# Performance work log

Measured on AMD Instinct MI355X. Metric: run time of the kernel, lower is better.

## Reference

```python
import jax, jax.numpy as jnp
import numpy as np

NUM_USERS = 100000
NUM_ITEMS = 200000
EMBED_DIM = 64
NUM_LAYERS = 3
NNZ = 4000000
BATCH = 16384
N_TOTAL = NUM_USERS + NUM_ITEMS


def setup_inputs() -> dict:
    key = jax.random.key(0)
    k = jax.random.split(key, 7)
    user_ids = jax.random.randint(k[0], (BATCH,), 0, NUM_USERS, dtype=jnp.int32)
    item_ids = jax.random.randint(k[1], (BATCH,), 0, NUM_ITEMS, dtype=jnp.int32)
    adj_row = jax.random.randint(k[2], (NNZ,), 0, N_TOTAL, dtype=jnp.int32)
    adj_col = jax.random.randint(k[3], (NNZ,), 0, N_TOTAL, dtype=jnp.int32)
    # normalized-adjacency-like positive values (D^-1/2 A D^-1/2 entries)
    adj_val = jax.random.uniform(k[4], (NNZ,), dtype=jnp.float32) * 0.1
    user_emb_w = jax.random.normal(k[5], (NUM_USERS, EMBED_DIM), dtype=jnp.float32) * 0.1
    item_emb_w = jax.random.normal(k[6], (NUM_ITEMS, EMBED_DIM), dtype=jnp.float32) * 0.1
    return {"user_ids": user_ids, "item_ids": item_ids, "adj_row": adj_row,
            "adj_col": adj_col, "adj_val": adj_val,
            "user_emb_w": user_emb_w, "item_emb_w": item_emb_w}


def _spmm(row, col, val, x):
    # y = A @ x for COO sparse A: gather source rows, scale, scatter-add to dest rows
    msgs = x[col] * val[:, None]  # [nnz, D]
    return jax.ops.segment_sum(msgs, row, num_segments=N_TOTAL)


def reference(user_ids, item_ids, adj_row, adj_col, adj_val, user_emb_w, item_emb_w):
    all_emb = jnp.concatenate([user_emb_w, item_emb_w], axis=0)  # [N+M, D]
    acc = all_emb  # running sum over K+1 layer embeddings (== stack+mean)
    x = all_emb
    for _ in range(NUM_LAYERS):
        x = _spmm(adj_row, adj_col, adj_val, x)
        acc = acc + x
    final = acc / jnp.float32(NUM_LAYERS + 1)
    u = final[user_ids]                    # [B, D]
    i = final[item_ids + NUM_USERS]        # [B, D]
    return jnp.sum(u * i, axis=-1)         # [B]
```

## Files before the change

### kernel.cpp

```cpp
#include <hip/hip_runtime.h>
#include <hip/hip_fp16.h>

#define NUM_USERS 100000
#define NUM_ITEMS 200000
#define NT        300000
#define D         64
#define NNZ_C     4000000
#define BATCH     16384

#define SB_LOG    10
#define SB_ROWS   1024
#define NSB       ((NT + SB_ROWS - 1) / SB_ROWS)
#define SBCAP     16384
#define CHUNK     8192
#define NCHUNK    ((NNZ_C + CHUNK - 1) / CHUNK)

__device__ inline void fma8(float4& a, float4& b, float v, uint4 g) {
    const __half2* h = (const __half2*)&g;
    float2 f0 = __half22float2(h[0]); a.x += v * f0.x; a.y += v * f0.y;
    float2 f1 = __half22float2(h[1]); a.z += v * f1.x; a.w += v * f1.y;
    float2 f2 = __half22float2(h[2]); b.x += v * f2.x; b.y += v * f2.y;
    float2 f3 = __half22float2(h[3]); b.z += v * f3.x; b.w += v * f3.y;
}

__device__ inline unsigned pack2(float x, float y) {
    __half2 h = __floats2half2_rn(x, y);
    return *(unsigned*)&h;
}

__global__ void p1_bin(const int* __restrict__ row, const int* __restrict__ col,
                       const float* __restrict__ val, int* __restrict__ bcnt,
                       int2* __restrict__ entries) {
    __shared__ int hist[NSB];
    __shared__ int cur[NSB];
    int tid = threadIdx.x;
    long cb = (long)blockIdx.x * CHUNK;
    int n = (int)((NNZ_C - cb < CHUNK) ? (NNZ_C - cb) : CHUNK);
    for (int i = tid; i < NSB; i += 512) hist[i] = 0;
    __syncthreads();
    for (int k = tid; k < n; k += 512)
        atomicAdd(&hist[row[cb + k] >> SB_LOG], 1);
    __syncthreads();
    for (int i = tid; i < NSB; i += 512)
        cur[i] = atomicAdd(&bcnt[i], hist[i]);
    __syncthreads();
    for (int k = tid; k < n; k += 512) {
        int r = row[cb + k];
        int b = r >> SB_LOG;
        int pos = atomicAdd(&cur[b], 1);
        if (pos < SBCAP)
            entries[(long)b * SBCAP + pos] =
                make_int2(col[cb + k] | ((r & (SB_ROWS - 1)) << 19),
                          __float_as_int(val[cb + k]));
    }
}

__global__ void bucket_scan(const int* __restrict__ bcnt, int* __restrict__ bucketstart,
                            int* __restrict__ rowstart) {
    __shared__ int s[512];
    int tid = threadIdx.x;
    int v = (tid < NSB) ? min(bcnt[tid], SBCAP) : 0;
    int acc = v;
    s[tid] = acc; __syncthreads();
    for (int off = 1; off < 512; off <<= 1) {
        int t = (tid >= off) ? s[tid - off] : 0;
        __syncthreads();
        acc += t; s[tid] = acc; __syncthreads();
    }
    if (tid < NSB) bucketstart[tid] = acc - v;
    if (tid == 0) rowstart[NT] = s[511];
}

__global__ void p2_csr(const int* __restrict__ bcnt, const int* __restrict__ bucketstart,
                       const int2* __restrict__ entries, int* __restrict__ rowstart,
                       int2* __restrict__ cv) {
    __shared__ int h[SB_ROWS];
    __shared__ int cur[SB_ROWS];
    int b = blockIdx.x, tid = threadIdx.x;
    int n = min(bcnt[b], SBCAP);
    const int2* eb = entries + (long)b * SBCAP;
    h[tid] = 0; __syncthreads();
    for (int k = tid; k < n; k += SB_ROWS)
        atomicAdd(&h[((unsigned)eb[k].x) >> 19], 1);
    __syncthreads();
    int v = h[tid];
    int acc = v;
    __syncthreads();
    for (int off = 1; off < SB_ROWS; off <<= 1) {
        int t = (tid >= off) ? h[tid - off] : 0;
        __syncthreads();
        acc += t; h[tid] = acc; __syncthreads();
    }
    int rs = bucketstart[b] + (acc - v);
    int grow = (b << SB_LOG) + tid;
    if (grow < NT) rowstart[grow] = rs;
    cur[tid] = rs;
    __syncthreads();
    for (int k = tid; k < n; k += SB_ROWS) {
        int2 e = eb[k];
        int rl = ((unsigned)e.x) >> 19;
        int p = atomicAdd(&cur[rl], 1);
        cv[p] = make_int2(e.x & 0x7FFFF, e.y);
    }
}

__global__ void mark_needed(const int* __restrict__ uid, const int* __restrict__ iid,
                            const int* __restrict__ rowstart, const int2* __restrict__ cv,
                            char* __restrict__ flags) {
    int t = blockIdx.x * blockDim.x + threadIdx.x;
    int r = (t < BATCH) ? uid[t] : (iid[t - BATCH] + NUM_USERS);
    flags[r] = 1;
    int e = rowstart[r + 1];
    for (int j = rowstart[r]; j < e; ++j)
        flags[cv[j].x] = 1;
}

__global__ void init_x0(const float* __restrict__ uw, const float* __restrict__ iw,
                        unsigned short* __restrict__ x0) {
    int t = blockIdx.x * blockDim.x + threadIdx.x;
    int r = t >> 3, sub = t & 7;
    const float* src = (r < NUM_USERS) ? (uw + (long)r * D)
                                       : (iw + (long)(r - NUM_USERS) * D);
    float4 f0 = ((const float4*)src)[sub * 2];
    float4 f1 = ((const float4*)src)[sub * 2 + 1];
    uint4 o;
    o.x = pack2(f0.x, f0.y); o.y = pack2(f0.z, f0.w);
    o.z = pack2(f1.x, f1.y); o.w = pack2(f1.z, f1.w);
    ((uint4*)(x0 + (long)r * D))[sub] = o;
}

template <bool FILT>
__global__ void csr_spmm_h(const int* __restrict__ rowstart, const int2* __restrict__ cv,
                           const unsigned short* __restrict__ x,
                           const char* __restrict__ flags,
                           unsigned short* __restrict__ y) {
    int r = blockIdx.x * 4 + (threadIdx.x >> 6);
    if (r >= NT) return;
    if (FILT && !flags[r]) return;
    int lane = threadIdx.x & 63;
    int grp = lane >> 3, sub = lane & 7;
    int s = rowstart[r], e = rowstart[r + 1];
    float4 a0 = make_float4(0.f, 0.f, 0.f, 0.f), a1 = a0;
    float4 b0 = a0, b1 = a0;
    for (int j = s; j < e; j += 16) {
        int i0 = j + grp, i1 = j + 8 + grp;
        int2 p0 = cv[(i0 < e) ? i0 : (e - 1)];
        int2 p1 = cv[(i1 < e) ? i1 : (e - 1)];
        float v0 = (i0 < e) ? __int_as_float(p0.y) : 0.f;
        float v1 = (i1 < e) ? __int_as_float(p1.y) : 0.f;
        uint4 g0 = *(const uint4*)(x + (long)p0.x * D + sub * 8);
        uint4 g1 = *(const uint4*)(x + (long)p1.x * D + sub * 8);
        fma8(a0, a1, v0, g0);
        fma8(b0, b1, v1, g1);
    }
    a0.x += b0.x; a0.y += b0.y; a0.z += b0.z; a0.w += b0.w;
    a1.x += b1.x; a1.y += b1.y; a1.z += b1.z; a1.w += b1.w;
    #pragma unroll
    for (int off = 8; off <= 32; off <<= 1) {
        a0.x += __shfl_xor(a0.x, off); a0.y += __shfl_xor(a0.y, off);
        a0.z += __shfl_xor(a0.z, off); a0.w += __shfl_xor(a0.w, off);
        a1.x += __shfl_xor(a1.x, off); a1.y += __shfl_xor(a1.y, off);
        a1.z += __shfl_xor(a1.z, off); a1.w += __shfl_xor(a1.w, off);
    }
    if (grp == 0) {
        uint4 o;
        o.x = pack2(a0.x, a0.y); o.y = pack2(a0.z, a0.w);
        o.z = pack2(a1.x, a1.y); o.w = pack2(a1.z, a1.w);
        ((uint4*)(y + (long)r * D))[sub] = o;
    }
}

__global__ void csr_spmm_acc_h(const int* __restrict__ uid, const int* __restrict__ iid,
                               const int* __restrict__ rowstart, const int2* __restrict__ cv,
                               const unsigned short* __restrict__ x,
                               float* __restrict__ acc) {
    int bidx = blockIdx.x * 4 + (threadIdx.x >> 6);
    if (bidx >= 2 * BATCH) return;
    int lane = threadIdx.x & 63;
    int grp = lane >> 3, sub = lane & 7;
    int r = (bidx < BATCH) ? uid[bidx] : (iid[bidx - BATCH] + NUM_USERS);
    int s = rowstart[r], e = rowstart[r + 1];
    float4 a0 = make_float4(0.f, 0.f, 0.f, 0.f), a1 = a0;
    float4 b0 = a0, b1 = a0;
    for (int j = s; j < e; j += 16) {
        int i0 = j + grp, i1 = j + 8 + grp;
        int2 p0 = cv[(i0 < e) ? i0 : (e - 1)];
        int2 p1 = cv[(i1 < e) ? i1 : (e - 1)];
        float v0 = (i0 < e) ? __int_as_float(p0.y) : 0.f;
        float v1 = (i1 < e) ? __int_as_float(p1.y) : 0.f;
        uint4 g0 = *(const uint4*)(x + (long)p0.x * D + sub * 8);
        uint4 g1 = *(const uint4*)(x + (long)p1.x * D + sub * 8);
        fma8(a0, a1, v0, g0);
        fma8(b0, b1, v1, g1);
    }
    a0.x += b0.x; a0.y += b0.y; a0.z += b0.z; a0.w += b0.w;
    a1.x += b1.x; a1.y += b1.y; a1.z += b1.z; a1.w += b1.w;
    #pragma unroll
    for (int off = 8; off <= 32; off <<= 1) {
        a0.x += __shfl_xor(a0.x, off); a0.y += __shfl_xor(a0.y, off);
        a0.z += __shfl_xor(a0.z, off); a0.w += __shfl_xor(a0.w, off);
        a1.x += __shfl_xor(a1.x, off); a1.y += __shfl_xor(a1.y, off);
        a1.z += __shfl_xor(a1.z, off); a1.w += __shfl_xor(a1.w, off);
    }
    if (grp == 0) {
        float4* ap = (float4*)(acc + (long)bidx * D) + sub * 2;
        float4 q0 = ap[0], q1 = ap[1];
        q0.x += a0.x; q0.y += a0.y; q0.z += a0.z; q0.w += a0.w;
        q1.x += a1.x; q1.y += a1.y; q1.z += a1.z; q1.w += a1.w;
        ap[0] = q0; ap[1] = q1;
    }
}

__global__ void gather_init(const int* __restrict__ uid, const int* __restrict__ iid,
                            const float* __restrict__ uw, const float* __restrict__ iw,
                            float* __restrict__ acc) {
    int t = blockIdx.x * blockDim.x + threadIdx.x;
    int b   = t >> 4;
    int sub = t & 15;
    const float* src = (b < BATCH) ? (uw + (long)uid[b] * D)
                                   : (iw + (long)iid[b - BATCH] * D);
    ((float4*)(acc + (long)b * D))[sub] = ((const float4*)src)[sub];
}

__global__ void gather_acc_h(const int* __restrict__ uid, const int* __restrict__ iid,
                             const unsigned short* __restrict__ x, float* __restrict__ acc) {
    int t = blockIdx.x * blockDim.x + threadIdx.x;
    int b   = t >> 3;
    int sub = t & 7;
    int r   = (b < BATCH) ? uid[b] : (iid[b - BATCH] + NUM_USERS);
    uint4 g = ((const uint4*)(x + (long)r * D))[sub];
    const __half2* h = (const __half2*)&g;
    float4* ap = (float4*)(acc + (long)b * D) + sub * 2;
    float4 q0 = ap[0], q1 = ap[1];
    float2 f0 = __half22float2(h[0]); q0.x += f0.x; q0.y += f0.y;
    float2 f1 = __half22float2(h[1]); q0.z += f1.x; q0.w += f1.y;
    float2 f2 = __half22float2(h[2]); q1.x += f2.x; q1.y += f2.y;
    float2 f3 = __half22float2(h[3]); q1.z += f3.x; q1.w += f3.y;
    ap[0] = q0; ap[1] = q1;
}

__global__ void final_dot(const float* __restrict__ acc, float* __restrict__ out) {
    int t = blockIdx.x * blockDim.x + threadIdx.x;
    int b   = t >> 4;
    int sub = t & 15;
    float4 u = *((const float4*)(acc + (long)b * D) + sub);
    float4 w = *((const float4*)(acc + (long)(b + BATCH) * D) + sub);
    float p = u.x * w.x + u.y * w.y + u.z * w.z + u.w * w.w;
    p += __shfl_xor(p, 1);
    p += __shfl_xor(p, 2);
    p += __shfl_xor(p, 4);
    p += __shfl_xor(p, 8);
    if (sub == 0) out[b] = p * (1.0f / 16.0f);
}

extern "C" void kernel_launch(void* const* d_in, const int* in_sizes, int n_in,
                              void* d_out, int out_size, void* d_ws, size_t ws_size,
                              hipStream_t stream) {
    const int*   user_ids = (const int*)d_in[0];
    const int*   item_ids = (const int*)d_in[1];
    const int*   adj_row  = (const int*)d_in[2];
    const int*   adj_col  = (const int*)d_in[3];
    const float* adj_val  = (const float*)d_in[4];
    const float* uw       = (const float*)d_in[5];
    const float* iw       = (const float*)d_in[6];
    float*       out      = (float*)d_out;

    char* ws = (char*)d_ws;
    size_t off = 0;
    auto alloc = [&](size_t bytes) {
        char* p = ws + off;
        off += (bytes + 255) & ~(size_t)255;
        return p;
    };
    const size_t xhbytes = (size_t)NT * D * sizeof(unsigned short);
    const size_t ebytes  = (size_t)NSB * SBCAP * sizeof(int2);
    unsigned short* x0h = (unsigned short*)alloc(xhbytes);
    unsigned short* xAh = (unsigned short*)alloc(xhbytes);
    unsigned short* xBh = (unsigned short*)alloc(ebytes > xhbytes ? ebytes : xhbytes);
    float* acc          = (float*)alloc((size_t)2 * BATCH * D * sizeof(float));
    int*   rowstart     = (int*)alloc((size_t)(NT + 1) * sizeof(int));
    int*   bcnt         = (int*)alloc((size_t)NSB * sizeof(int));
    int*   bucketstart  = (int*)alloc((size_t)NSB * sizeof(int));
    char*  flags        = (char*)alloc((size_t)NT);
    int2*  cv           = (int2*)alloc((size_t)NNZ_C * sizeof(int2));
    int2*  entries      = (int2*)xBh;

    hipMemsetAsync(bcnt, 0, (size_t)NSB * sizeof(int), stream);
    p1_bin<<<NCHUNK, 512, 0, stream>>>(adj_row, adj_col, adj_val, bcnt, entries);
    bucket_scan<<<1, 512, 0, stream>>>(bcnt, bucketstart, rowstart);
    p2_csr<<<NSB, SB_ROWS, 0, stream>>>(bcnt, bucketstart, entries, rowstart, cv);

    hipMemsetAsync(flags, 0, (size_t)NT, stream);
    mark_needed<<<(2 * BATCH) / 256, 256, 0, stream>>>(user_ids, item_ids, rowstart, cv, flags);

    init_x0<<<(NT * 8) / 256, 256, 0, stream>>>(uw, iw, x0h);
    gather_init<<<(2 * BATCH * 16) / 256, 256, 0, stream>>>(user_ids, item_ids, uw, iw, acc);

    csr_spmm_h<false><<<(NT + 3) / 4, 256, 0, stream>>>(rowstart, cv, x0h, nullptr, xAh);
    gather_acc_h<<<(2 * BATCH * 8) / 256, 256, 0, stream>>>(user_ids, item_ids, xAh, acc);

    csr_spmm_h<true><<<(NT + 3) / 4, 256, 0, stream>>>(rowstart, cv, xAh, flags, xBh);
    gather_acc_h<<<(2 * BATCH * 8) / 256, 256, 0, stream>>>(user_ids, item_ids, xBh, acc);

    csr_spmm_acc_h<<<(2 * BATCH + 3) / 4, 256, 0, stream>>>(user_ids, item_ids,
                                                            rowstart, cv, xBh, acc);

    final_dot<<<(BATCH * 16) / 256, 256, 0, stream>>>(acc, out);
}
```

Before: 511.6 us.

## Pad CSR rows to multiples of 16 with fixed bucket strides and use fma_mix

```diff
diff --git a/kernel.cpp b/kernel.cpp
--- a/kernel.cpp
+++ b/kernel.cpp
@@ -12,20 +12,28 @@
 #define SB_ROWS   1024
 #define NSB       ((NT + SB_ROWS - 1) / SB_ROWS)
 #define SBCAP     16384
+#define BSTRIDE   24576
 #define CHUNK     8192
 #define NCHUNK    ((NNZ_C + CHUNK - 1) / CHUNK)
-
-__device__ inline void fma8(float4& a, float4& b, float v, uint4 g) {
-    const __half2* h = (const __half2*)&g;
-    float2 f0 = __half22float2(h[0]); a.x += v * f0.x; a.y += v * f0.y;
-    float2 f1 = __half22float2(h[1]); a.z += v * f1.x; a.w += v * f1.y;
-    float2 f2 = __half22float2(h[2]); b.x += v * f2.x; b.y += v * f2.y;
-    float2 f3 = __half22float2(h[3]); b.z += v * f3.x; b.w += v * f3.y;
-}
 
 __device__ inline unsigned pack2(float x, float y) {
     __half2 h = __floats2half2_rn(x, y);
     return *(unsigned*)&h;
+}
+
+__device__ inline void fma_mix8(float4& a, float4& b, uint4 g, float v) {
+    asm("v_fma_mix_f32 %0, %2, %3, %0 op_sel:[0,0,0] op_sel_hi:[1,0,0]\n\t"
+        "v_fma_mix_f32 %1, %2, %3, %1 op_sel:[1,0,0] op_sel_hi:[1,0,0]"
+        : "+v"(a.x), "+v"(a.y) : "v"(g.x), "v"(v));
+    asm("v_fma_mix_f32 %0, %2, %3, %0 op_sel:[0,0,0] op_sel_hi:[1,0,0]\n\t"
+        "v_fma_mix_f32 %1, %2, %3, %1 op_sel:[1,0,0] op_sel_hi:[1,0,0]"
+        : "+v"(a.z), "+v"(a.w) : "v"(g.y), "v"(v));
+    asm("v_fma_mix_f32 %0, %2, %3, %0 op_sel:[0,0,0] op_sel_hi:[1,0,0]\n\t"
+        "v_fma_mix_f32 %1, %2, %3, %1 op_sel:[1,0,0] op_sel_hi:[1,0,0]"
+        : "+v"(b.x), "+v"(b.y) : "v"(g.z), "v"(v));
+    asm("v_fma_mix_f32 %0, %2, %3, %0 op_sel:[0,0,0] op_sel_hi:[1,0,0]\n\t"
+        "v_fma_mix_f32 %1, %2, %3, %1 op_sel:[1,0,0] op_sel_hi:[1,0,0]"
+        : "+v"(b.z), "+v"(b.w) : "v"(g.w), "v"(v));
 }
 
 __global__ void p1_bin(const int* __restrict__ row, const int* __restrict__ col,
@@ -55,24 +63,8 @@
     }
 }
 
-__global__ void bucket_scan(const int* __restrict__ bcnt, int* __restrict__ bucketstart,
-                            int* __restrict__ rowstart) {
-    __shared__ int s[512];
-    int tid = threadIdx.x;
-    int v = (tid < NSB) ? min(bcnt[tid], SBCAP) : 0;
-    int acc = v;
-    s[tid] = acc; __syncthreads();
-    for (int off = 1; off < 512; off <<= 1) {
-        int t = (tid >= off) ? s[tid - off] : 0;
-        __syncthreads();
-        acc += t; s[tid] = acc; __syncthreads();
-    }
-    if (tid < NSB) bucketstart[tid] = acc - v;
-    if (tid == 0) rowstart[NT] = s[511];
-}
-
-__global__ void p2_csr(const int* __restrict__ bcnt, const int* __restrict__ bucketstart,
-                       const int2* __restrict__ entries, int* __restrict__ rowstart,
+__global__ void p2_csr(const int* __restrict__ bcnt, const int2* __restrict__ entries,
+                       int* __restrict__ rowstart, int* __restrict__ rowend,
                        int2* __restrict__ cv) {
     __shared__ int h[SB_ROWS];
     __shared__ int cur[SB_ROWS];
@@ -83,17 +75,19 @@
     for (int k = tid; k < n; k += SB_ROWS)
         atomicAdd(&h[((unsigned)eb[k].x) >> 19], 1);
     __syncthreads();
-    int v = h[tid];
-    int acc = v;
+    int raw = h[tid];
+    int pad = (raw + 15) & ~15;
+    h[tid] = pad;
+    int acc = pad;
     __syncthreads();
     for (int off = 1; off < SB_ROWS; off <<= 1) {
         int t = (tid >= off) ? h[tid - off] : 0;
         __syncthreads();
         acc += t; h[tid] = acc; __syncthreads();
     }
-    int rs = bucketstart[b] + (acc - v);
+    int rs = b * BSTRIDE + (acc - pad);
     int grow = (b << SB_LOG) + tid;
-    if (grow < NT) rowstart[grow] = rs;
+    if (grow < NT) { rowstart[grow] = rs; rowend[grow] = rs + pad; }
     cur[tid] = rs;
     __syncthreads();
     for (int k = tid; k < n; k += SB_ROWS) {
@@ -102,15 +96,17 @@
         int p = atomicAdd(&cur[rl], 1);
         cv[p] = make_int2(e.x & 0x7FFFF, e.y);
     }
+    for (int p = rs + raw; p < rs + pad; ++p)
+        cv[p] = make_int2(0, 0);
 }
 
 __global__ void mark_needed(const int* __restrict__ uid, const int* __restrict__ iid,
-                            const int* __restrict__ rowstart, const int2* __restrict__ cv,
-                            char* __restrict__ flags) {
+                            const int* __restrict__ rowstart, const int* __restrict__ rowend,
+                            const int2* __restrict__ cv, char* __restrict__ flags) {
     int t = blockIdx.x * blockDim.x + threadIdx.x;
     int r = (t < BATCH) ? uid[t] : (iid[t - BATCH] + NUM_USERS);
     flags[r] = 1;
-    int e = rowstart[r + 1];
+    int e = rowend[r];
     for (int j = rowstart[r]; j < e; ++j)
         flags[cv[j].x] = 1;
 }
@@ -130,28 +126,24 @@
 }
 
 template <bool FILT>
-__global__ void csr_spmm_h(const int* __restrict__ rowstart, const int2* __restrict__ cv,
-                           const unsigned short* __restrict__ x,
-                           const char* __restrict__ flags,
-                           unsigned short* __restrict__ y) {
+__global__ void csr_spmm_h(const int* __restrict__ rowstart, const int* __restrict__ rowend,
+                           const int2* __restrict__ cv, const unsigned short* __restrict__ x,
+                           const char* __restrict__ flags, unsigned short* __restrict__ y) {
     int r = blockIdx.x * 4 + (threadIdx.x >> 6);
     if (r >= NT) return;
     if (FILT && !flags[r]) return;
     int lane = threadIdx.x & 63;
     int grp = lane >> 3, sub = lane & 7;
-    int s = rowstart[r], e = rowstart[r + 1];
-    float4 a0 = make_float4(0.f, 0.f, 0.f, 0.f), a1 = a0;
-    float4 b0 = a0, b1 = a0;
-    for (int j = s; j < e; j += 16) {
-        int i0 = j + grp, i1 = j + 8 + grp;
-        int2 p0 = cv[(i0 < e) ? i0 : (e - 1)];
-        int2 p1 = cv[(i1 < e) ? i1 : (e - 1)];
-        float v0 = (i0 < e) ? __int_as_float(p0.y) : 0.f;
-        float v1 = (i1 < e) ? __int_as_float(p1.y) : 0.f;
-        uint4 g0 = *(const uint4*)(x + (long)p0.x * D + sub * 8);
-        uint4 g1 = *(const uint4*)(x + (long)p1.x * D + sub * 8);
-        fma8(a0, a1, v0, g0);
-        fma8(b0, b1, v1, g1);
+    int s = rowstart[r], e = rowend[r];
+    const unsigned short* xs = x + sub * 8;
+    float4 a0 = make_float4(0.f, 0.f, 0.f, 0.f), a1 = a0, b0 = a0, b1 = a0;
+    for (int j = s + grp; j < e; j += 16) {
+        int2 p0 = cv[j];
+        int2 p1 = cv[j + 8];
+        uint4 g0 = *(const uint4*)(xs + (long)p0.x * D);
+        uint4 g1 = *(const uint4*)(xs + (long)p1.x * D);
+        fma_mix8(a0, a1, g0, __int_as_float(p0.y));
+        fma_mix8(b0, b1, g1, __int_as_float(p1.y));
     }
     a0.x += b0.x; a0.y += b0.y; a0.z += b0.z; a0.w += b0.w;
     a1.x += b1.x; a1.y += b1.y; a1.z += b1.z; a1.w += b1.w;
@@ -171,7 +163,8 @@
 }
 
 __global__ void csr_spmm_acc_h(const int* __restrict__ uid, const int* __restrict__ iid,
-                               const int* __restrict__ rowstart, const int2* __restrict__ cv,
+                               const int* __restrict__ rowstart, const int* __restrict__ rowend,
+                               const int2* __restrict__ cv,
                                const unsigned short* __restrict__ x,
                                float* __restrict__ acc) {
     int bidx = blockIdx.x * 4 + (threadIdx.x >> 6);
@@ -179,19 +172,16 @@
     int lane = threadIdx.x & 63;
     int grp = lane >> 3, sub = lane & 7;
     int r = (bidx < BATCH) ? uid[bidx] : (iid[bidx - BATCH] + NUM_USERS);
-    int s = rowstart[r], e = rowstart[r + 1];
-    float4 a0 = make_float4(0.f, 0.f, 0.f, 0.f), a1 = a0;
-    float4 b0 = a0, b1 = a0;
-    for (int j = s; j < e; j += 16) {
-        int i0 = j + grp, i1 = j + 8 + grp;
-        int2 p0 = cv[(i0 < e) ? i0 : (e - 1)];
-        int2 p1 = cv[(i1 < e) ? i1 : (e - 1)];
-        float v0 = (i0 < e) ? __int_as_float(p0.y) : 0.f;
-        float v1 = (i1 < e) ? __int_as_float(p1.y) : 0.f;
-        uint4 g0 = *(const uint4*)(x + (long)p0.x * D + sub * 8);
-        uint4 g1 = *(const uint4*)(x + (long)p1.x * D + sub * 8);
-        fma8(a0, a1, v0, g0);
-        fma8(b0, b1, v1, g1);
+    int s = rowstart[r], e = rowend[r];
+    const unsigned short* xs = x + sub * 8;
+    float4 a0 = make_float4(0.f, 0.f, 0.f, 0.f), a1 = a0, b0 = a0, b1 = a0;
+    for (int j = s + grp; j < e; j += 16) {
+        int2 p0 = cv[j];
+        int2 p1 = cv[j + 8];
+        uint4 g0 = *(const uint4*)(xs + (long)p0.x * D);
+        uint4 g1 = *(const uint4*)(xs + (long)p1.x * D);
+        fma_mix8(a0, a1, g0, __int_as_float(p0.y));
+        fma_mix8(b0, b1, g1, __int_as_float(p1.y));
     }
     a0.x += b0.x; a0.y += b0.y; a0.z += b0.z; a0.w += b0.w;
     a1.x += b1.x; a1.y += b1.y; a1.z += b1.z; a1.w += b1.w;
@@ -278,32 +268,32 @@
     unsigned short* xAh = (unsigned short*)alloc(xhbytes);
     unsigned short* xBh = (unsigned short*)alloc(ebytes > xhbytes ? ebytes : xhbytes);
     float* acc          = (float*)alloc((size_t)2 * BATCH * D * sizeof(float));
-    int*   rowstart     = (int*)alloc((size_t)(NT + 1) * sizeof(int));
+    int*   rowstart     = (int*)alloc((size_t)NT * sizeof(int));
+    int*   rowend       = (int*)alloc((size_t)NT * sizeof(int));
     int*   bcnt         = (int*)alloc((size_t)NSB * sizeof(int));
-    int*   bucketstart  = (int*)alloc((size_t)NSB * sizeof(int));
     char*  flags        = (char*)alloc((size_t)NT);
-    int2*  cv           = (int2*)alloc((size_t)NNZ_C * sizeof(int2));
+    int2*  cv           = (int2*)alloc((size_t)NSB * BSTRIDE * sizeof(int2));
     int2*  entries      = (int2*)xBh;
 
     hipMemsetAsync(bcnt, 0, (size_t)NSB * sizeof(int), stream);
     p1_bin<<<NCHUNK, 512, 0, stream>>>(adj_row, adj_col, adj_val, bcnt, entries);
-    bucket_scan<<<1, 512, 0, stream>>>(bcnt, bucketstart, rowstart);
-    p2_csr<<<NSB, SB_ROWS, 0, stream>>>(bcnt, bucketstart, entries, rowstart, cv);
+    p2_csr<<<NSB, SB_ROWS, 0, stream>>>(bcnt, entries, rowstart, rowend, cv);
 
     hipMemsetAsync(flags, 0, (size_t)NT, stream);
-    mark_needed<<<(2 * BATCH) / 256, 256, 0, stream>>>(user_ids, item_ids, rowstart, cv, flags);
+    mark_needed<<<(2 * BATCH) / 256, 256, 0, stream>>>(user_ids, item_ids, rowstart, rowend,
+                                                       cv, flags);
 
     init_x0<<<(NT * 8) / 256, 256, 0, stream>>>(uw, iw, x0h);
     gather_init<<<(2 * BATCH * 16) / 256, 256, 0, stream>>>(user_ids, item_ids, uw, iw, acc);
 
-    csr_spmm_h<false><<<(NT + 3) / 4, 256, 0, stream>>>(rowstart, cv, x0h, nullptr, xAh);
+    csr_spmm_h<false><<<(NT + 3) / 4, 256, 0, stream>>>(rowstart, rowend, cv, x0h, nullptr, xAh);
     gather_acc_h<<<(2 * BATCH * 8) / 256, 256, 0, stream>>>(user_ids, item_ids, xAh, acc);
 
-    csr_spmm_h<true><<<(NT + 3) / 4, 256, 0, stream>>>(rowstart, cv, xAh, flags, xBh);
+    csr_spmm_h<true><<<(NT + 3) / 4, 256, 0, stream>>>(rowstart, rowend, cv, xAh, flags, xBh);
     gather_acc_h<<<(2 * BATCH * 8) / 256, 256, 0, stream>>>(user_ids, item_ids, xBh, acc);
 
     csr_spmm_acc_h<<<(2 * BATCH + 3) / 4, 256, 0, stream>>>(user_ids, item_ids,
-                                                            rowstart, cv, xBh, acc);
+                                                            rowstart, rowend, cv, xBh, acc);
 
     final_dot<<<(BATCH * 16) / 256, 256, 0, stream>>>(acc, out);
 }
```

Result: no change. 510.4 us (-0.2%).
